# Kernel optimization log

Measured on AMD Instinct MI355X. Metric: run time of the kernel, lower is better.

## Reference

```python
import jax, jax.numpy as jnp
import numpy as np

H = 512
B, LQ, LA = 16, 64, 100


def setup_inputs() -> dict:
    key = jax.random.key(0)
    ks = jax.random.split(key, 10)
    s = 1.0 / np.sqrt(H)
    return {
        "content1": jax.random.normal(ks[0], (B, LQ, H), dtype=jnp.float32),
        "content2": jax.random.normal(ks[1], (B, LA, H), dtype=jnp.float32),
        "is_user": 0,
        "W_q": jax.random.normal(ks[2], (H, H), dtype=jnp.float32) * s,
        "b_q": jax.random.normal(ks[3], (H,), dtype=jnp.float32) * s,
        "W_a": jax.random.normal(ks[4], (H, H), dtype=jnp.float32) * s,
        "b_a": jax.random.normal(ks[5], (H,), dtype=jnp.float32) * s,
        "W_aq": jax.random.normal(ks[6], (H, H), dtype=jnp.float32) * s,
        "b_aq": jax.random.normal(ks[7], (H,), dtype=jnp.float32) * s,
        "W_v": jax.random.normal(ks[8], (H, 1), dtype=jnp.float32) * s,
        "b_v": jax.random.normal(ks[9], (1,), dtype=jnp.float32) * s,
    }


def _entropy(x, axis):
    logp = jax.nn.log_softmax(x, axis=axis)
    p = jnp.exp(logp)
    return -1.0 * jnp.sum(p * logp, axis=axis)


def reference(content1, content2, is_user, W_q, b_q, W_a, b_a, W_aq, b_aq, W_v, b_v):
    # Branch is_user==0 (question x answer mutual attention).
    # Original expands content1 to [B,Lq,La,H] and content2 to [B,Lq,La,H];
    # since the three linears are applied to values constant along the
    # broadcast axes, we project pre-expansion (same math, less FLOPs).
    # m = tanh(w_a_m(c1) + w_q_m(c2) + w_aq_m(c1*c1))  (c1*c1 as in source)
    a1 = content1 @ W_a + b_a + (content1 * content1) @ W_aq + b_aq  # [B,Lq,H]
    q2 = content2 @ W_q + b_q                                        # [B,La,H]
    m = jnp.tanh(a1[:, :, None, :] + q2[:, None, :, :])              # [B,Lq,La,H]
    score = m @ W_v + b_v                                            # [B,Lq,La,1]
    beta = _entropy(score, axis=2)                                   # [B,Lq,1]
    return beta
```

## Files before the change

### kernel.cpp

```cpp
#include <hip/hip_runtime.h>
#include <math.h>

#define H    512
#define LQ   64
#define LA   100
#define LAP  128
#define L2E2 2.885390081777927f

using short8  = __attribute__((ext_vector_type(8))) short;
using floatx4 = __attribute__((ext_vector_type(4))) float;

__device__ __forceinline__ unsigned short f2bf(float f) {
    unsigned int u = __float_as_uint(f);
    u += 0x7fffu + ((u >> 16) & 1u);
    return (unsigned short)(u >> 16);
}
__device__ __forceinline__ unsigned int packbf2(float a, float b) {
    return (unsigned int)f2bf(a) | ((unsigned int)f2bf(b) << 16);
}

__global__ __launch_bounds__(256) void prep_kernel(
    const float* __restrict__ Wq, const float* __restrict__ Wa,
    const float* __restrict__ Waq,
    unsigned short* __restrict__ B1T, unsigned short* __restrict__ B2T)
{
    __shared__ float lt[64][65];
    const int bid = blockIdx.x;
    const int mat = bid >> 6;
    const int tile = bid & 63;
    const int k0 = (tile >> 3) * 64, n0 = (tile & 7) * 64;
    const float* W = (mat == 0) ? Wa : (mat == 1) ? Waq : Wq;
    const int t = threadIdx.x;
#pragma unroll
    for (int i = 0; i < 16; ++i) {
        int idx = i * 256 + t;
        int k = idx >> 6, n = idx & 63;
        lt[n][k] = W[(size_t)(k0 + k) * H + n0 + n];
    }
    __syncthreads();
    unsigned short* dst; int Kt, koff;
    if (mat == 2) { dst = B2T; Kt = 512;  koff = k0; }
    else          { dst = B1T; Kt = 1024; koff = k0 + (mat == 1 ? 512 : 0); }
#pragma unroll
    for (int i = 0; i < 8; ++i) {
        int idx = i * 256 + t;
        int n = idx >> 5, kk = (idx & 31) * 2;
        unsigned int p = packbf2(lt[n][kk], lt[n][kk + 1]);
        *(unsigned int*)(dst + (size_t)(n0 + n) * Kt + koff + kk) = p;
    }
}

__global__ __launch_bounds__(256) void gemm_kernel(
    const float* __restrict__ c1, const float* __restrict__ c2,
    const unsigned short* __restrict__ B1T, const unsigned short* __restrict__ B2T,
    const float* __restrict__ bq, const float* __restrict__ ba,
    const float* __restrict__ baq,
    float* __restrict__ a1, float* __restrict__ q2t)
{
    __shared__ __align__(16) unsigned short As[64 * 64];
    __shared__ __align__(16) unsigned short Bs[64 * 64];

    const int bid = blockIdx.x;
    const bool g1 = bid < 128;
    int mt, nt, Ktot;
    if (g1) { mt = bid >> 3; nt = bid & 7; Ktot = 1024; }
    else { int b2 = bid - 128; mt = b2 >> 3; nt = b2 & 7; Ktot = 512; }
    const int m0 = mt * 64, n0 = nt * 64;
    const unsigned short* BT = g1 ? B1T : B2T;

    const int t = threadIdx.x;
    const int w = t >> 6, lane = t & 63;
    const int q = lane >> 4, ln = lane & 15;
    const int sm = t >> 2, sc = t & 3;

    floatx4 acc[4];
#pragma unroll
    for (int j = 0; j < 4; ++j) acc[j] = (floatx4){0.f, 0.f, 0.f, 0.f};

    for (int k0 = 0; k0 < Ktot; k0 += 64) {
        __syncthreads();
        {
            const bool sq = g1 && (k0 >= 512);
            const float* X = g1 ? c1 : c2;
            const float* src = X + (size_t)(m0 + sm) * H
                                 + (k0 - (sq ? 512 : 0)) + sc * 16;
            float4 f0 = *(const float4*)(src);
            float4 f1 = *(const float4*)(src + 4);
            float4 f2 = *(const float4*)(src + 8);
            float4 f3 = *(const float4*)(src + 12);
            if (sq) {
                f0.x *= f0.x; f0.y *= f0.y; f0.z *= f0.z; f0.w *= f0.w;
                f1.x *= f1.x; f1.y *= f1.y; f1.z *= f1.z; f1.w *= f1.w;
                f2.x *= f2.x; f2.y *= f2.y; f2.z *= f2.z; f2.w *= f2.w;
                f3.x *= f3.x; f3.y *= f3.y; f3.z *= f3.z; f3.w *= f3.w;
            }
            uint4 p0, p1;
            p0.x = packbf2(f0.x, f0.y); p0.y = packbf2(f0.z, f0.w);
            p0.z = packbf2(f1.x, f1.y); p0.w = packbf2(f1.z, f1.w);
            p1.x = packbf2(f2.x, f2.y); p1.y = packbf2(f2.z, f2.w);
            p1.z = packbf2(f3.x, f3.y); p1.w = packbf2(f3.z, f3.w);
            const int c = sc * 2, sw = sm & 7;
            *(uint4*)((char*)As + sm * 128 + ((c    ) ^ sw) * 16) = p0;
            *(uint4*)((char*)As + sm * 128 + ((c + 1) ^ sw) * 16) = p1;
        }
        {
            const unsigned short* src = BT + (size_t)(n0 + sm) * Ktot + k0 + sc * 16;
            uint4 q0 = *(const uint4*)(src);
            uint4 q1 = *(const uint4*)(src + 8);
            const int c = sc * 2, sw = sm & 7;
            *(uint4*)((char*)Bs + sm * 128 + ((c    ) ^ sw) * 16) = q0;
            *(uint4*)((char*)Bs + sm * 128 + ((c + 1) ^ sw) * 16) = q1;
        }
        __syncthreads();
#pragma unroll
        for (int s = 0; s < 2; ++s) {
            const int off = ((s * 4 + q) ^ (ln & 7)) * 16;
            short8 af = *(const short8*)((const char*)As + (w * 16 + ln) * 128 + off);
#pragma unroll
            for (int j = 0; j < 4; ++j) {
                short8 bf = *(const short8*)((const char*)Bs + (j * 16 + ln) * 128 + off);
                acc[j] = __builtin_amdgcn_mfma_f32_16x16x32_bf16(af, bf, acc[j], 0, 0, 0);
            }
        }
    }

    if (g1) {
#pragma unroll
        for (int j = 0; j < 4; ++j) {
            const int N = n0 + j * 16 + ln;
            const float bias = ba[N] + baq[N];
#pragma unroll
            for (int r = 0; r < 4; ++r) {
                const int R = m0 + w * 16 + q * 4 + r;
                a1[(size_t)R * H + N] = (acc[j][r] + bias) * L2E2;
            }
        }
    } else {
#pragma unroll
        for (int r = 0; r < 4; ++r) {
            const int R = m0 + w * 16 + q * 4 + r;
            const int bb = (R * 5243) >> 19;
            const int aa = R - bb * 100;
            float* dst = q2t + (size_t)bb * (H * LAP) + aa;
#pragma unroll
            for (int j = 0; j < 4; ++j) {
                const int N = n0 + j * 16 + ln;
                dst[(size_t)N * LAP] = (acc[j][r] + bq[N]) * L2E2;
            }
        }
    }
}

__global__ __launch_bounds__(1024) void score_entropy_kernel(
    const float* __restrict__ a1, const float* __restrict__ q2t,
    const float* __restrict__ wvp, const float* __restrict__ bvp,
    float* __restrict__ out)
{
    __shared__ __align__(16) float a1s[4][H];
    __shared__ __align__(16) float wvs[H];
    __shared__ __align__(16) float part[8][LAP][4];

    const int t  = threadIdx.x;
    const int b  = blockIdx.x >> 4;
    const int qg = blockIdx.x & 15;

    for (int i = t; i < 4 * H; i += 1024) {
        int q = i >> 9, h = i & (H - 1);
        a1s[q][h] = a1[(size_t)(b * LQ + (qg << 2) + q) * H + h];
    }
    if (t < H) wvs[t] = wvp[t];
    __syncthreads();

    const int a  = t & 127;
    const int hh = t >> 7;
    const int hb = hh * 64;
    const float* q2p = q2t + (size_t)b * (H * LAP) + (size_t)hb * LAP + a;

    float R0 = 0.f, R1 = 0.f, R2 = 0.f, R3 = 0.f;
#pragma unroll 8
    for (int h = 0; h < 64; ++h) {
        float v = q2p[(size_t)h * LAP];
        float w = wvs[hb + h];
        float r0 = __builtin_amdgcn_rcpf(__builtin_amdgcn_exp2f(a1s[0][hb + h] + v) + 1.f);
        float r1 = __builtin_amdgcn_rcpf(__builtin_amdgcn_exp2f(a1s[1][hb + h] + v) + 1.f);
        float r2 = __builtin_amdgcn_rcpf(__builtin_amdgcn_exp2f(a1s[2][hb + h] + v) + 1.f);
        float r3 = __builtin_amdgcn_rcpf(__builtin_amdgcn_exp2f(a1s[3][hb + h] + v) + 1.f);
        R0 = fmaf(w, r0, R0);
        R1 = fmaf(w, r1, R1);
        R2 = fmaf(w, r2, R2);
        R3 = fmaf(w, r3, R3);
    }
    *(float4*)(&part[hh][a][0]) = make_float4(R0, R1, R2, R3);
    __syncthreads();

    if (t < 256) {
        const int l = t & 63, q = t >> 6;
        float ws = 0.f;
#pragma unroll
        for (int i = 0; i < 8; ++i) ws += wvs[l + (i << 6)];
#pragma unroll
        for (int o = 32; o; o >>= 1) ws += __shfl_xor(ws, o);

        const float base = bvp[0] + ws;
        float s1 = 0.f, s2 = 0.f;
#pragma unroll
        for (int i = 0; i < 8; ++i) s1 += part[i][l][q];
        const bool act2 = l < (LA - 64);
        if (act2) {
#pragma unroll
            for (int i = 0; i < 8; ++i) s2 += part[i][l + 64][q];
        }
        float sc1 = base - 2.f * s1;
        float sc2 = act2 ? (base - 2.f * s2) : -INFINITY;
        float m = fmaxf(sc1, sc2);
#pragma unroll
        for (int o = 32; o; o >>= 1) m = fmaxf(m, __shfl_xor(m, o));

        const float L2E = 1.4426950408889634f;
        float e1 = __builtin_amdgcn_exp2f((sc1 - m) * L2E);
        float e2 = act2 ? __builtin_amdgcn_exp2f((sc2 - m) * L2E) : 0.f;
        float Z = e1 + e2;
        float S = e1 * sc1 + (act2 ? e2 * sc2 : 0.f);
#pragma unroll
        for (int o = 32; o; o >>= 1) {
            Z += __shfl_xor(Z, o);
            S += __shfl_xor(S, o);
        }
        if (l == 0) out[b * LQ + (qg << 2) + q] = m + logf(Z) - S / Z;
    }
}

extern "C" void kernel_launch(void* const* d_in, const int* in_sizes, int n_in,
                              void* d_out, int out_size, void* d_ws, size_t ws_size,
                              hipStream_t stream) {
    const float* c1  = (const float*)d_in[0];
    const float* c2  = (const float*)d_in[1];
    const float* Wq  = (const float*)d_in[3];
    const float* bq  = (const float*)d_in[4];
    const float* Wa  = (const float*)d_in[5];
    const float* ba  = (const float*)d_in[6];
    const float* Waq = (const float*)d_in[7];
    const float* baq = (const float*)d_in[8];
    const float* Wv  = (const float*)d_in[9];
    const float* bv  = (const float*)d_in[10];
    float* out = (float*)d_out;

    float* a1  = (float*)d_ws;
    float* q2t = a1 + (size_t)1024 * 512;
    unsigned short* B1T = (unsigned short*)(q2t + (size_t)16 * 512 * 128);
    unsigned short* B2T = B1T + (size_t)512 * 1024;

    prep_kernel<<<dim3(192), dim3(256), 0, stream>>>(Wq, Wa, Waq, B1T, B2T);
    gemm_kernel<<<dim3(328), dim3(256), 0, stream>>>(c1, c2, B1T, B2T,
                                                     bq, ba, baq, a1, q2t);
    score_entropy_kernel<<<dim3(256), dim3(1024), 0, stream>>>(a1, q2t, Wv, bv, out);
}
```

Baseline: 115.8 us.

## Pre-tile bf16 swizzled operands and double-buffer GEMM with async LDS loads

The prep kernel now converts c1 (plus its square), c2 and the weights into pre-swizzled 64x64 bf16 tiles in workspace. The GEMM can then stream whole tiles straight into LDS with global_load_lds into a double buffer, overlapping the next tile's load with MFMA on the current one and dropping the per-tile conversion from the GEMM. The score kernel also loads its LDS operands as float4 and processes four h values per iteration. The cost is an extra workspace round trip for the activations and a larger prep grid.

```diff
diff --git a/kernel.cpp b/kernel.cpp
--- a/kernel.cpp
+++ b/kernel.cpp
@@ -19,109 +19,143 @@
     return (unsigned int)f2bf(a) | ((unsigned int)f2bf(b) << 16);
 }
 
+__device__ __forceinline__ void async_cp16(const void* g, void* l) {
+    __builtin_amdgcn_global_load_lds(
+        (const __attribute__((address_space(1))) unsigned int*)(uintptr_t)g,
+        (__attribute__((address_space(3))) unsigned int*)(unsigned int)(uintptr_t)l,
+        16, 0, 0);
+}
+
 __global__ __launch_bounds__(256) void prep_kernel(
+    const float* __restrict__ c1, const float* __restrict__ c2,
     const float* __restrict__ Wq, const float* __restrict__ Wa,
     const float* __restrict__ Waq,
-    unsigned short* __restrict__ B1T, unsigned short* __restrict__ B2T)
+    unsigned short* __restrict__ A1sw, unsigned short* __restrict__ A2sw,
+    unsigned short* __restrict__ B1sw, unsigned short* __restrict__ B2sw)
 {
-    __shared__ float lt[64][65];
-    const int bid = blockIdx.x;
-    const int mat = bid >> 6;
-    const int tile = bid & 63;
-    const int k0 = (tile >> 3) * 64, n0 = (tile & 7) * 64;
-    const float* W = (mat == 0) ? Wa : (mat == 1) ? Waq : Wq;
-    const int t = threadIdx.x;
-#pragma unroll
-    for (int i = 0; i < 16; ++i) {
-        int idx = i * 256 + t;
-        int k = idx >> 6, n = idx & 63;
-        lt[n][k] = W[(size_t)(k0 + k) * H + n0 + n];
-    }
-    __syncthreads();
-    unsigned short* dst; int Kt, koff;
-    if (mat == 2) { dst = B2T; Kt = 512;  koff = k0; }
-    else          { dst = B1T; Kt = 1024; koff = k0 + (mat == 1 ? 512 : 0); }
-#pragma unroll
-    for (int i = 0; i < 8; ++i) {
-        int idx = i * 256 + t;
-        int n = idx >> 5, kk = (idx & 31) * 2;
-        unsigned int p = packbf2(lt[n][kk], lt[n][kk + 1]);
-        *(unsigned int*)(dst + (size_t)(n0 + n) * Kt + koff + kk) = p;
+    __shared__ __align__(16) float lt[64][68];
+    const int bid = blockIdx.x, t = threadIdx.x;
+
+    if (bid < 328) {
+        const bool isA1 = bid < 128;
+        int mt, kc; const float* X;
+        if (isA1) { mt = bid >> 3; kc = bid & 7; X = c1; }
+        else      { int b2 = bid - 128; mt = b2 >> 3; kc = b2 & 7; X = c2; }
+#pragma unroll
+        for (int i = 0; i < 4; ++i) {
+            int idx = i * 256 + t;
+            int r = idx >> 4, c4 = idx & 15;
+            float4 v = *(const float4*)(X + (size_t)(mt * 64 + r) * H + kc * 64 + c4 * 4);
+            int bytepos = r * 128 + (((c4 >> 1) ^ (r & 7)) * 16) + (c4 & 1) * 8;
+            if (isA1) {
+                unsigned short* t1 = A1sw + (size_t)(mt * 16 + kc) * 4096;
+                *(uint2*)((char*)t1 + bytepos) = make_uint2(packbf2(v.x, v.y), packbf2(v.z, v.w));
+                unsigned short* t2 = A1sw + (size_t)(mt * 16 + kc + 8) * 4096;
+                *(uint2*)((char*)t2 + bytepos) =
+                    make_uint2(packbf2(v.x * v.x, v.y * v.y), packbf2(v.z * v.z, v.w * v.w));
+            } else {
+                unsigned short* t1 = A2sw + (size_t)(mt * 8 + kc) * 4096;
+                *(uint2*)((char*)t1 + bytepos) = make_uint2(packbf2(v.x, v.y), packbf2(v.z, v.w));
+            }
+        }
+    } else {
+        int b3 = bid - 328;
+        const bool isB1 = b3 < 128;
+        int nt, kc; const float* W; int k0;
+        if (isB1) { nt = b3 >> 4; kc = b3 & 15; W = (kc < 8) ? Wa : Waq; k0 = (kc & 7) * 64; }
+        else      { int b4 = b3 - 128; nt = b4 >> 3; kc = b4 & 7; W = Wq; k0 = kc * 64; }
+        const int n0 = nt * 64;
+#pragma unroll
+        for (int i = 0; i < 4; ++i) {
+            int idx = i * 256 + t;
+            int k = idx >> 4, n4 = idx & 15;
+            float4 v = *(const float4*)(W + (size_t)(k0 + k) * H + n0 + n4 * 4);
+            lt[n4 * 4 + 0][k] = v.x;
+            lt[n4 * 4 + 1][k] = v.y;
+            lt[n4 * 4 + 2][k] = v.z;
+            lt[n4 * 4 + 3][k] = v.w;
+        }
+        __syncthreads();
+#pragma unroll
+        for (int i = 0; i < 4; ++i) {
+            int idx = i * 256 + t;
+            int r = idx >> 4, c4 = idx & 15;
+            float4 v = *(const float4*)&lt[r][c4 * 4];
+            int bytepos = r * 128 + (((c4 >> 1) ^ (r & 7)) * 16) + (c4 & 1) * 8;
+            unsigned short* tile = isB1 ? B1sw + (size_t)(nt * 16 + kc) * 4096
+                                        : B2sw + (size_t)(nt * 8 + kc) * 4096;
+            *(uint2*)((char*)tile + bytepos) = make_uint2(packbf2(v.x, v.y), packbf2(v.z, v.w));
+        }
     }
 }
 
 __global__ __launch_bounds__(256) void gemm_kernel(
-    const float* __restrict__ c1, const float* __restrict__ c2,
-    const unsigned short* __restrict__ B1T, const unsigned short* __restrict__ B2T,
+    const unsigned short* __restrict__ A1sw, const unsigned short* __restrict__ A2sw,
+    const unsigned short* __restrict__ B1sw, const unsigned short* __restrict__ B2sw,
     const float* __restrict__ bq, const float* __restrict__ ba,
     const float* __restrict__ baq,
     float* __restrict__ a1, float* __restrict__ q2t)
 {
-    __shared__ __align__(16) unsigned short As[64 * 64];
-    __shared__ __align__(16) unsigned short Bs[64 * 64];
+    __shared__ __align__(16) unsigned short As[2][4096];
+    __shared__ __align__(16) unsigned short Bs[2][4096];
 
     const int bid = blockIdx.x;
     const bool g1 = bid < 128;
-    int mt, nt, Ktot;
-    if (g1) { mt = bid >> 3; nt = bid & 7; Ktot = 1024; }
-    else { int b2 = bid - 128; mt = b2 >> 3; nt = b2 & 7; Ktot = 512; }
+    int mt, nt, nk;
+    const unsigned short *Abase, *Bbase;
+    if (g1) {
+        mt = bid >> 3; nt = bid & 7; nk = 16;
+        Abase = A1sw + (size_t)(mt * 16) * 4096;
+        Bbase = B1sw + (size_t)(nt * 16) * 4096;
+    } else {
+        int b2 = bid - 128; mt = b2 >> 3; nt = b2 & 7; nk = 8;
+        Abase = A2sw + (size_t)(mt * 8) * 4096;
+        Bbase = B2sw + (size_t)(nt * 8) * 4096;
+    }
     const int m0 = mt * 64, n0 = nt * 64;
-    const unsigned short* BT = g1 ? B1T : B2T;
 
     const int t = threadIdx.x;
     const int w = t >> 6, lane = t & 63;
     const int q = lane >> 4, ln = lane & 15;
-    const int sm = t >> 2, sc = t & 3;
+    const int goff = w * 1024 + lane * 8;
+    const int loff = w * 1024;
 
     floatx4 acc[4];
 #pragma unroll
     for (int j = 0; j < 4; ++j) acc[j] = (floatx4){0.f, 0.f, 0.f, 0.f};
 
-    for (int k0 = 0; k0 < Ktot; k0 += 64) {
-        __syncthreads();
-        {
-            const bool sq = g1 && (k0 >= 512);
-            const float* X = g1 ? c1 : c2;
-            const float* src = X + (size_t)(m0 + sm) * H
-                                 + (k0 - (sq ? 512 : 0)) + sc * 16;
-            float4 f0 = *(const float4*)(src);
-            float4 f1 = *(const float4*)(src + 4);
-            float4 f2 = *(const float4*)(src + 8);
-            float4 f3 = *(const float4*)(src + 12);
-            if (sq) {
-                f0.x *= f0.x; f0.y *= f0.y; f0.z *= f0.z; f0.w *= f0.w;
-                f1.x *= f1.x; f1.y *= f1.y; f1.z *= f1.z; f1.w *= f1.w;
-                f2.x *= f2.x; f2.y *= f2.y; f2.z *= f2.z; f2.w *= f2.w;
-                f3.x *= f3.x; f3.y *= f3.y; f3.z *= f3.z; f3.w *= f3.w;
-            }
-            uint4 p0, p1;
-            p0.x = packbf2(f0.x, f0.y); p0.y = packbf2(f0.z, f0.w);
-            p0.z = packbf2(f1.x, f1.y); p0.w = packbf2(f1.z, f1.w);
-            p1.x = packbf2(f2.x, f2.y); p1.y = packbf2(f2.z, f2.w);
-            p1.z = packbf2(f3.x, f3.y); p1.w = packbf2(f3.z, f3.w);
-            const int c = sc * 2, sw = sm & 7;
-            *(uint4*)((char*)As + sm * 128 + ((c    ) ^ sw) * 16) = p0;
-            *(uint4*)((char*)As + sm * 128 + ((c + 1) ^ sw) * 16) = p1;
-        }
-        {
-            const unsigned short* src = BT + (size_t)(n0 + sm) * Ktot + k0 + sc * 16;
-            uint4 q0 = *(const uint4*)(src);
-            uint4 q1 = *(const uint4*)(src + 8);
-            const int c = sc * 2, sw = sm & 7;
-            *(uint4*)((char*)Bs + sm * 128 + ((c    ) ^ sw) * 16) = q0;
-            *(uint4*)((char*)Bs + sm * 128 + ((c + 1) ^ sw) * 16) = q1;
-        }
-        __syncthreads();
+    {
+        const unsigned short* ga = Abase;
+        const unsigned short* gb = Bbase;
+        async_cp16(ga + goff,       &As[0][loff]);
+        async_cp16(ga + goff + 512, &As[0][loff + 512]);
+        async_cp16(gb + goff,       &Bs[0][loff]);
+        async_cp16(gb + goff + 512, &Bs[0][loff + 512]);
+    }
+    __syncthreads();
+
+    int buf = 0;
+    for (int kc = 0; kc < nk; ++kc) {
+        if (kc + 1 < nk) {
+            const unsigned short* ga = Abase + (size_t)(kc + 1) * 4096;
+            const unsigned short* gb = Bbase + (size_t)(kc + 1) * 4096;
+            async_cp16(ga + goff,       &As[buf ^ 1][loff]);
+            async_cp16(ga + goff + 512, &As[buf ^ 1][loff + 512]);
+            async_cp16(gb + goff,       &Bs[buf ^ 1][loff]);
+            async_cp16(gb + goff + 512, &Bs[buf ^ 1][loff + 512]);
+        }
 #pragma unroll
         for (int s = 0; s < 2; ++s) {
             const int off = ((s * 4 + q) ^ (ln & 7)) * 16;
-            short8 af = *(const short8*)((const char*)As + (w * 16 + ln) * 128 + off);
+            short8 af = *(const short8*)((const char*)&As[buf][0] + (w * 16 + ln) * 128 + off);
 #pragma unroll
             for (int j = 0; j < 4; ++j) {
-                short8 bf = *(const short8*)((const char*)Bs + (j * 16 + ln) * 128 + off);
+                short8 bf = *(const short8*)((const char*)&Bs[buf][0] + (j * 16 + ln) * 128 + off);
                 acc[j] = __builtin_amdgcn_mfma_f32_16x16x32_bf16(af, bf, acc[j], 0, 0, 0);
             }
         }
+        __syncthreads();
+        buf ^= 1;
     }
 
     if (g1) {
@@ -177,19 +211,30 @@
     const float* q2p = q2t + (size_t)b * (H * LAP) + (size_t)hb * LAP + a;
 
     float R0 = 0.f, R1 = 0.f, R2 = 0.f, R3 = 0.f;
-#pragma unroll 8
-    for (int h = 0; h < 64; ++h) {
-        float v = q2p[(size_t)h * LAP];
-        float w = wvs[hb + h];
-        float r0 = __builtin_amdgcn_rcpf(__builtin_amdgcn_exp2f(a1s[0][hb + h] + v) + 1.f);
-        float r1 = __builtin_amdgcn_rcpf(__builtin_amdgcn_exp2f(a1s[1][hb + h] + v) + 1.f);
-        float r2 = __builtin_amdgcn_rcpf(__builtin_amdgcn_exp2f(a1s[2][hb + h] + v) + 1.f);
-        float r3 = __builtin_amdgcn_rcpf(__builtin_amdgcn_exp2f(a1s[3][hb + h] + v) + 1.f);
-        R0 = fmaf(w, r0, R0);
-        R1 = fmaf(w, r1, R1);
-        R2 = fmaf(w, r2, R2);
-        R3 = fmaf(w, r3, R3);
-    }
+#define TERM(Rq, Aq, vv, ww) \
+    Rq = fmaf(ww, __builtin_amdgcn_rcpf(__builtin_amdgcn_exp2f((Aq) + (vv)) + 1.f), Rq)
+#pragma unroll 4
+    for (int i = 0; i < 16; ++i) {
+        const int h4 = i * 4;
+        float4 wv4 = *(const float4*)&wvs[hb + h4];
+        float4 A0 = *(const float4*)&a1s[0][hb + h4];
+        float4 A1 = *(const float4*)&a1s[1][hb + h4];
+        float4 A2 = *(const float4*)&a1s[2][hb + h4];
+        float4 A3 = *(const float4*)&a1s[3][hb + h4];
+        float v0 = q2p[(size_t)(h4 + 0) * LAP];
+        float v1 = q2p[(size_t)(h4 + 1) * LAP];
+        float v2 = q2p[(size_t)(h4 + 2) * LAP];
+        float v3 = q2p[(size_t)(h4 + 3) * LAP];
+        TERM(R0, A0.x, v0, wv4.x); TERM(R0, A0.y, v1, wv4.y);
+        TERM(R0, A0.z, v2, wv4.z); TERM(R0, A0.w, v3, wv4.w);
+        TERM(R1, A1.x, v0, wv4.x); TERM(R1, A1.y, v1, wv4.y);
+        TERM(R1, A1.z, v2, wv4.z); TERM(R1, A1.w, v3, wv4.w);
+        TERM(R2, A2.x, v0, wv4.x); TERM(R2, A2.y, v1, wv4.y);
+        TERM(R2, A2.z, v2, wv4.z); TERM(R2, A2.w, v3, wv4.w);
+        TERM(R3, A3.x, v0, wv4.x); TERM(R3, A3.y, v1, wv4.y);
+        TERM(R3, A3.z, v2, wv4.z); TERM(R3, A3.w, v3, wv4.w);
+    }
+#undef TERM
     *(float4*)(&part[hh][a][0]) = make_float4(R0, R1, R2, R3);
     __syncthreads();
 
@@ -247,11 +292,14 @@
 
     float* a1  = (float*)d_ws;
     float* q2t = a1 + (size_t)1024 * 512;
-    unsigned short* B1T = (unsigned short*)(q2t + (size_t)16 * 512 * 128);
-    unsigned short* B2T = B1T + (size_t)512 * 1024;
-
-    prep_kernel<<<dim3(192), dim3(256), 0, stream>>>(Wq, Wa, Waq, B1T, B2T);
-    gemm_kernel<<<dim3(328), dim3(256), 0, stream>>>(c1, c2, B1T, B2T,
+    unsigned short* A1sw = (unsigned short*)(q2t + (size_t)16 * 512 * 128);
+    unsigned short* A2sw = A1sw + (size_t)16 * 16 * 4096;
+    unsigned short* B1sw = A2sw + (size_t)25 * 8 * 4096;
+    unsigned short* B2sw = B1sw + (size_t)8 * 16 * 4096;
+
+    prep_kernel<<<dim3(520), dim3(256), 0, stream>>>(c1, c2, Wq, Wa, Waq,
+                                                     A1sw, A2sw, B1sw, B2sw);
+    gemm_kernel<<<dim3(328), dim3(256), 0, stream>>>(A1sw, A2sw, B1sw, B2sw,
                                                      bq, ba, baq, a1, q2t);
     score_entropy_kernel<<<dim3(256), dim3(1024), 0, stream>>>(a1, q2t, Wv, bv, out);
 }
```

Result: faster. 105.9 us (-8.6%).
